# Performance work log

Hardware: AMD Instinct MI355X
Metric: run time of the kernel (lower is better)

The kernel has to match this reference:

```python
import jax, jax.numpy as jnp
import numpy as np

B, H, L, P = 16, 256, 4096, 64  # batch, d_input, seq len (= kernel_size), d_state
R_MIN, R_MAX = 0.9, 1.0         # strong_stability, weak_stability (discrete reservoir radii)


def _as_complex(x):
    # torch.view_as_complex equivalent: trailing dim 2 = (real, imag)
    return x[..., 0] + 1j * x[..., 1]


def setup_inputs() -> dict:
    key = jax.random.key(0)
    ks = jax.random.split(key, 6)
    u = jax.random.normal(ks[0], (B, H, L), jnp.float32)
    C = jax.random.normal(ks[1], (H, P, 2), jnp.float32)       # complex (H,P) as view_as_real
    D = jax.random.normal(ks[2], (H, H), jnp.float32)
    B_bar = jax.random.normal(ks[3], (P, H, 2), jnp.float32)   # complex (P,H) as view_as_real
    # DiscreteStateReservoir: eigenvalues with |lambda| in [strong, weak), uniform phase
    radius = jax.random.uniform(ks[4], (P,), jnp.float32, R_MIN, R_MAX)
    theta = jax.random.uniform(ks[5], (P,), jnp.float32, 0.0, 2.0 * np.pi)
    Lambda_bar = jnp.stack([radius * jnp.cos(theta), radius * jnp.sin(theta)], axis=-1)
    powers = jnp.arange(L, dtype=jnp.float32)
    return {"u": u, "C": C, "D": D, "B_bar": B_bar, "Lambda_bar": Lambda_bar, "powers": powers}


def reference(u, C, D, B_bar, Lambda_bar, powers):
    Cc = _as_complex(C)            # (H, P) complex64
    Bc = _as_complex(B_bar)        # (P, H) complex64
    Lc = _as_complex(Lambda_bar)   # (P,)   complex64
    # Vandermonde: (P, L) = Lambda_bar[p] ** powers[l]
    vand = Lc[:, None] ** powers[None, :]
    # einsum('hp,ph->hp') is elementwise C[h,p]*B_bar[p,h]; then contract over p
    kernel = jnp.einsum('hp,pl->hl', Cc * Bc.T, vand)            # (H, L) complex64
    # circular FFT convolution along L
    y = jnp.fft.ifft(jnp.fft.fft(u, axis=-1) * jnp.fft.fft(kernel, axis=-1)[None], axis=-1)
    # einsum('hh,bhl->bhl', D, u) uses only diag(D)
    y = y.real + jnp.diagonal(D)[None, :, None] * u
    return jnp.tanh(y)
```

## Files before the change

### kernel.cpp

```cpp
#include <hip/hip_runtime.h>
#include <cmath>

#define NF 4096
#define PI2F 6.2831853071795864769f

typedef float2 cf;

__device__ __forceinline__ cf cmulf(cf a, cf b){
  return make_float2(fmaf(a.x, b.x, -(a.y*b.y)), fmaf(a.x, b.y, a.y*b.x));
}
__device__ __forceinline__ cf cadd(cf a, cf b){ return make_float2(a.x+b.x, a.y+b.y); }
__device__ __forceinline__ cf csub(cf a, cf b){ return make_float2(a.x-b.x, a.y-b.y); }

__device__ __forceinline__ int phys8(int i){ return i + (i >> 3); }

__device__ __forceinline__ int rev8(int i){
  return ((i & 7) << 9) | (((i >> 3) & 7) << 6) | (((i >> 6) & 7) << 3) | ((i >> 9) & 7);
}

template<int INV>
__device__ __forceinline__ void dft8(cf* v){
  const float HF = 0.7071067811865476f;
  cf e0,e1,e2,e3,o0,o1,o2,o3;
  {
    cf t0 = cadd(v[0], v[4]);
    cf t1 = csub(v[0], v[4]);
    cf t2 = cadd(v[2], v[6]);
    cf t3 = csub(v[2], v[6]);
    e0 = cadd(t0,t2); e2 = csub(t0,t2);
    if (!INV){ e1 = make_float2(t1.x+t3.y, t1.y-t3.x); e3 = make_float2(t1.x-t3.y, t1.y+t3.x); }
    else     { e1 = make_float2(t1.x-t3.y, t1.y+t3.x); e3 = make_float2(t1.x+t3.y, t1.y-t3.x); }
  }
  {
    cf t0 = cadd(v[1], v[5]);
    cf t1 = csub(v[1], v[5]);
    cf t2 = cadd(v[3], v[7]);
    cf t3 = csub(v[3], v[7]);
    o0 = cadd(t0,t2); o2 = csub(t0,t2);
    if (!INV){ o1 = make_float2(t1.x+t3.y, t1.y-t3.x); o3 = make_float2(t1.x-t3.y, t1.y+t3.x); }
    else     { o1 = make_float2(t1.x-t3.y, t1.y+t3.x); o3 = make_float2(t1.x+t3.y, t1.y-t3.x); }
  }
  cf w1, w2, w3;
  if (!INV){
    w1 = make_float2(HF*(o1.x + o1.y), HF*(o1.y - o1.x));
    w2 = make_float2(o2.y, -o2.x);
    w3 = make_float2(HF*(o3.y - o3.x), -HF*(o3.x + o3.y));
  } else {
    w1 = make_float2(HF*(o1.x - o1.y), HF*(o1.y + o1.x));
    w2 = make_float2(-o2.y, o2.x);
    w3 = make_float2(-HF*(o3.x + o3.y), HF*(o3.x - o3.y));
  }
  v[0] = cadd(e0,o0); v[4] = csub(e0,o0);
  v[1] = cadd(e1,w1); v[5] = csub(e1,w1);
  v[2] = cadd(e2,w2); v[6] = csub(e2,w2);
  v[3] = cadd(e3,w3); v[7] = csub(e3,w3);
}

__device__ __forceinline__ void twiddle8(cf* v, float ang){
  float s, c;
  __sincosf(ang, &s, &c);
  float c2 = 2.0f * c;
  cf T[8];
  T[1] = make_float2(c, s);
  T[2] = make_float2(fmaf(c2, c, -1.0f), c2 * s);
#pragma unroll
  for (int r = 3; r < 8; ++r)
    T[r] = make_float2(fmaf(c2, T[r-1].x, -T[r-2].x), fmaf(c2, T[r-1].y, -T[r-2].y));
#pragma unroll
  for (int r = 1; r < 8; ++r) v[r] = cmulf(v[r], T[r]);
}

__device__ __forceinline__ float fast_tanh(float x){
  float e = __expf(2.0f*x);
  return 1.0f - __fdividef(2.0f, e + 1.0f);
}

__global__ void k_geo(const float* __restrict__ Lam, float4* __restrict__ tab){
  int gid = blockIdx.x*256 + threadIdx.x;
  int p = gid >> 12;
  int w = gid & 4095;
  int k = rev8(w);
  double lr = (double)Lam[2*p], li = (double)Lam[2*p+1];
  double r2 = lr*lr + li*li;
  double r  = sqrt(r2);
  double tt = atan2(li, lr) * 0.15915494309189535;
  double rN = exp2(4096.0 * (0.5 * log2(r2)));
  double pN = 4096.0 * tt;
  pN -= floor(pN);
  double sN, cN;
  sincospi(2.0*pN, &sN, &cN);
  double numr = 1.0 - rN*cN;
  double numi =     - rN*sN;
  double ph1 = tt - (double)k * (1.0/4096.0);
  double s1, c1; sincospi(2.0*ph1, &s1, &c1);
  double d1r = 1.0 - r*c1, d1i = -r*s1;
  double inv1 = 1.0/(d1r*d1r + d1i*d1i);
  double g1r = (numr*d1r + numi*d1i)*inv1;
  double g1i = (numi*d1r - numr*d1i)*inv1;
  double ph2 = tt + (double)k * (1.0/4096.0);
  double s2, c2; sincospi(2.0*ph2, &s2, &c2);
  double d2r = 1.0 - r*c2, d2i = -r*s2;
  double inv2 = 1.0/(d2r*d2r + d2i*d2i);
  double g2r = (numr*d2r + numi*d2i)*inv2;
  double g2i = (numi*d2r - numr*d2i)*inv2;
  const double hN = 0.5/4096.0;
  double Ar  =  (g1r + g2r)*hN, Ai  = (g1i - g2i)*hN;
  double B2r = -(g1i + g2i)*hN, B2i = (g1r - g2r)*hN;
  tab[(size_t)p*4096 + w] = make_float4((float)Ar, (float)Ai, (float)B2r, (float)B2i);
}

__global__ __launch_bounds__(512,4) void k_red(
    const float* __restrict__ C, const float* __restrict__ Bb,
    const float4* __restrict__ tab, const float* __restrict__ D,
    cf* __restrict__ M){
  __shared__ cf Wsh[32][64];
  __shared__ float4 Tt[8][128];
  const int t  = threadIdx.x;
  const int hg = blockIdx.x >> 5;
  const int ls = blockIdx.x & 31;
  const int h0 = hg*32;
  const int w0 = ls*128;
#pragma unroll
  for (int e = 0; e < 4; ++e){
    int idx = e*512 + t;
    int hl = idx >> 6, p = idx & 63;
    int h = h0 + hl;
    cf cc = ((const cf*)C)[h*64 + p];
    cf bb = ((const cf*)Bb)[p*256 + h];
    Wsh[hl][p] = cmulf(cc, bb);
  }
  const int wave = t >> 6;
  const int lane = t & 63;
  const int hh = wave*4;
  float accr[2][4] = {{0,0,0,0},{0,0,0,0}};
  float acci[2][4] = {{0,0,0,0},{0,0,0,0}};
  for (int pc = 0; pc < 8; ++pc){
    __syncthreads();
#pragma unroll
    for (int e = 0; e < 2; ++e){
      int idx = e*512 + t;
      int row = idx >> 7, col = idx & 127;
      Tt[row][col] = tab[(size_t)(pc*8 + row)*4096 + w0 + col];
    }
    __syncthreads();
#pragma unroll
    for (int p = 0; p < 8; ++p){
      cf Wc[4];
#pragma unroll
      for (int h = 0; h < 4; ++h) Wc[h] = Wsh[hh + h][pc*8 + p];
#pragma unroll
      for (int j = 0; j < 2; ++j){
        float4 f = Tt[p][lane + 64*j];
#pragma unroll
        for (int h = 0; h < 4; ++h){
          accr[j][h] = fmaf(Wc[h].x, f.x, fmaf(Wc[h].y, f.z, accr[j][h]));
          acci[j][h] = fmaf(Wc[h].x, f.y, fmaf(Wc[h].y, f.w, acci[j][h]));
        }
      }
    }
  }
  const float invN = 1.0f/4096.0f;
#pragma unroll
  for (int h = 0; h < 4; ++h){
    int hq = h0 + hh + h;
    float dd = D[hq*256 + hq] * invN;
#pragma unroll
    for (int j = 0; j < 2; ++j)
      M[(size_t)hq*NF + w0 + lane + 64*j] = make_float2(accr[j][h] + dd, acci[j][h]);
  }
}

__global__ __launch_bounds__(512,8) void k_main(
    const float* __restrict__ u, const cf* __restrict__ M, float* __restrict__ out){
  __shared__ cf X[4608];
  const int t  = threadIdx.x;
  const int h  = blockIdx.x >> 3;
  const int pr = blockIdx.x & 7;
  const size_t row0 = ((size_t)pr*256 + h)*(size_t)NF;
  const size_t row1 = row0 + (size_t)8*256*NF;
  const float* u0 = u + row0;
  const float* u1 = u + row1;
  cf v[8];
#pragma unroll
  for (int q = 0; q < 8; ++q) v[q] = make_float2(u0[t + 512*q], u1[t + 512*q]);
  dft8<0>(v);
  twiddle8(v, -(PI2F/4096.0f)*(float)t);
#pragma unroll
  for (int r = 0; r < 8; ++r) X[phys8(t + 512*r)] = v[r];
  __syncthreads();
  const int b2 = ((t >> 6) << 9) | (t & 63);
#pragma unroll
  for (int q = 0; q < 8; ++q) v[q] = X[phys8(b2 + 64*q)];
  dft8<0>(v);
  twiddle8(v, -(PI2F/512.0f)*(float)(t & 63));
#pragma unroll
  for (int r = 0; r < 8; ++r) X[phys8(b2 + 64*r)] = v[r];
  __syncthreads();
  const int b3 = ((t >> 3) << 6) | (t & 7);
#pragma unroll
  for (int q = 0; q < 8; ++q) v[q] = X[phys8(b3 + 8*q)];
  dft8<0>(v);
  twiddle8(v, -(PI2F/64.0f)*(float)(t & 7));
#pragma unroll
  for (int r = 0; r < 8; ++r) X[phys8(b3 + 8*r)] = v[r];
  __syncthreads();
  float4 mf0, mf1;
  {
    const float4* Mr = (const float4*)(M + (size_t)h*NF + 8*t);
    mf0 = Mr[0]; mf1 = Mr[1];
  }
#pragma unroll
  for (int q = 0; q < 8; ++q) v[q] = X[phys8(8*t + q)];
  dft8<0>(v);
  {
    const float4* Mr = (const float4*)(M + (size_t)h*NF + 8*t);
    float4 f2 = Mr[2], f3 = Mr[3];
    v[0] = cmulf(v[0], make_float2(mf0.x, mf0.y));
    v[1] = cmulf(v[1], make_float2(mf0.z, mf0.w));
    v[2] = cmulf(v[2], make_float2(mf1.x, mf1.y));
    v[3] = cmulf(v[3], make_float2(mf1.z, mf1.w));
    v[4] = cmulf(v[4], make_float2(f2.x, f2.y));
    v[5] = cmulf(v[5], make_float2(f2.z, f2.w));
    v[6] = cmulf(v[6], make_float2(f3.x, f3.y));
    v[7] = cmulf(v[7], make_float2(f3.z, f3.w));
  }
  dft8<1>(v);
#pragma unroll
  for (int q = 0; q < 8; ++q) X[phys8(8*t + q)] = v[q];
  __syncthreads();
#pragma unroll
  for (int r = 0; r < 8; ++r) v[r] = X[phys8(b3 + 8*r)];
  twiddle8(v, (PI2F/64.0f)*(float)(t & 7));
  dft8<1>(v);
#pragma unroll
  for (int q = 0; q < 8; ++q) X[phys8(b3 + 8*q)] = v[q];
  __syncthreads();
#pragma unroll
  for (int r = 0; r < 8; ++r) v[r] = X[phys8(b2 + 64*r)];
  twiddle8(v, (PI2F/512.0f)*(float)(t & 63));
  dft8<1>(v);
#pragma unroll
  for (int q = 0; q < 8; ++q) X[phys8(b2 + 64*q)] = v[q];
  __syncthreads();
#pragma unroll
  for (int r = 0; r < 8; ++r) v[r] = X[phys8(t + 512*r)];
  twiddle8(v, (PI2F/4096.0f)*(float)t);
  dft8<1>(v);
  float* o0 = out + row0;
  float* o1 = out + row1;
#pragma unroll
  for (int q = 0; q < 8; ++q){
    o0[t + 512*q] = fast_tanh(v[q].x);
    o1[t + 512*q] = fast_tanh(v[q].y);
  }
}

extern "C" void kernel_launch(void* const* d_in, const int* in_sizes, int n_in,
                              void* d_out, int out_size, void* d_ws, size_t ws_size,
                              hipStream_t stream){
  const float* u   = (const float*)d_in[0];
  const float* C   = (const float*)d_in[1];
  const float* D   = (const float*)d_in[2];
  const float* Bb  = (const float*)d_in[3];
  const float* Lam = (const float*)d_in[4];
  float* out = (float*)d_out;
  char* ws = (char*)d_ws;
  cf*     M   = (cf*)ws;
  float4* tab = (float4*)(ws + (size_t)(8u << 20));

  k_geo <<<dim3(1024), dim3(256), 0, stream>>>(Lam, tab);
  k_red <<<dim3(256),  dim3(512), 0, stream>>>(C, Bb, tab, D, M);
  k_main<<<dim3(2048), dim3(512), 0, stream>>>(u, M, out);
}
```

Measured before the change: 64.04 us.

## Compute geometric table in float with per-block shared setup; prefetch M early

```diff
diff --git a/kernel.cpp b/kernel.cpp
--- a/kernel.cpp
+++ b/kernel.cpp
@@ -75,38 +75,45 @@
   return 1.0f - __fdividef(2.0f, e + 1.0f);
 }
 
-__global__ void k_geo(const float* __restrict__ Lam, float4* __restrict__ tab){
-  int gid = blockIdx.x*256 + threadIdx.x;
-  int p = gid >> 12;
-  int w = gid & 4095;
-  int k = rev8(w);
-  double lr = (double)Lam[2*p], li = (double)Lam[2*p+1];
-  double r2 = lr*lr + li*li;
-  double r  = sqrt(r2);
-  double tt = atan2(li, lr) * 0.15915494309189535;
-  double rN = exp2(4096.0 * (0.5 * log2(r2)));
-  double pN = 4096.0 * tt;
-  pN -= floor(pN);
-  double sN, cN;
-  sincospi(2.0*pN, &sN, &cN);
-  double numr = 1.0 - rN*cN;
-  double numi =     - rN*sN;
-  double ph1 = tt - (double)k * (1.0/4096.0);
-  double s1, c1; sincospi(2.0*ph1, &s1, &c1);
-  double d1r = 1.0 - r*c1, d1i = -r*s1;
-  double inv1 = 1.0/(d1r*d1r + d1i*d1i);
-  double g1r = (numr*d1r + numi*d1i)*inv1;
-  double g1i = (numi*d1r - numr*d1i)*inv1;
-  double ph2 = tt + (double)k * (1.0/4096.0);
-  double s2, c2; sincospi(2.0*ph2, &s2, &c2);
-  double d2r = 1.0 - r*c2, d2i = -r*s2;
-  double inv2 = 1.0/(d2r*d2r + d2i*d2i);
-  double g2r = (numr*d2r + numi*d2i)*inv2;
-  double g2i = (numi*d2r - numr*d2i)*inv2;
-  const double hN = 0.5/4096.0;
-  double Ar  =  (g1r + g2r)*hN, Ai  = (g1i - g2i)*hN;
-  double B2r = -(g1i + g2i)*hN, B2i = (g1r - g2r)*hN;
-  tab[(size_t)p*4096 + w] = make_float4((float)Ar, (float)Ai, (float)B2r, (float)B2i);
+__global__ __launch_bounds__(1024) void k_geo(const float* __restrict__ Lam,
+                                              float4* __restrict__ tab){
+  __shared__ float sh[4];
+  const int p = blockIdx.x;
+  const int t = threadIdx.x;
+  if (t == 0){
+    double lr = (double)Lam[2*p], li = (double)Lam[2*p+1];
+    double r2 = lr*lr + li*li;
+    double tt = atan2(li, lr) * 0.15915494309189535;
+    double rN = exp2(4096.0 * (0.5 * log2(r2)));
+    double pN = 4096.0 * tt;  pN -= floor(pN);
+    double sN, cN;  sincospi(2.0*pN, &sN, &cN);
+    sh[0] = (float)tt;
+    sh[1] = (float)sqrt(r2);
+    sh[2] = (float)(1.0 - rN*cN);
+    sh[3] = (float)(-rN*sN);
+  }
+  __syncthreads();
+  const float tt = sh[0], r = sh[1], numr = sh[2], numi = sh[3];
+  const float hN = 0.5f/4096.0f;
+  float4* dst = tab + (size_t)p*4096;
+#pragma unroll
+  for (int s = 0; s < 4; ++s){
+    int w = s*1024 + t;
+    int k = rev8(w);
+    float kf = (float)k * (1.0f/4096.0f);
+    float s1, c1;  sincospif(2.0f*(tt - kf), &s1, &c1);
+    float d1r = fmaf(-r, c1, 1.0f), d1i = -r*s1;
+    float i1 = 1.0f / fmaf(d1r, d1r, d1i*d1i);
+    float g1r = (numr*d1r + numi*d1i)*i1;
+    float g1i = (numi*d1r - numr*d1i)*i1;
+    float s2, c2;  sincospif(2.0f*(tt + kf), &s2, &c2);
+    float d2r = fmaf(-r, c2, 1.0f), d2i = -r*s2;
+    float i2 = 1.0f / fmaf(d2r, d2r, d2i*d2i);
+    float g2r = (numr*d2r + numi*d2i)*i2;
+    float g2i = (numi*d2r - numr*d2i)*i2;
+    dst[w] = make_float4( (g1r + g2r)*hN, (g1i - g2i)*hN,
+                         -(g1i + g2i)*hN, (g1r - g2r)*hN);
+  }
 }
 
 __global__ __launch_bounds__(512,4) void k_red(
@@ -183,6 +190,8 @@
   cf v[8];
 #pragma unroll
   for (int q = 0; q < 8; ++q) v[q] = make_float2(u0[t + 512*q], u1[t + 512*q]);
+  const float4* Mr = (const float4*)(M + (size_t)h*NF + 8*t);
+  float4 mf0 = Mr[0], mf1 = Mr[1], mf2 = Mr[2], mf3 = Mr[3];
   dft8<0>(v);
   twiddle8(v, -(PI2F/4096.0f)*(float)t);
 #pragma unroll
@@ -204,26 +213,17 @@
 #pragma unroll
   for (int r = 0; r < 8; ++r) X[phys8(b3 + 8*r)] = v[r];
   __syncthreads();
-  float4 mf0, mf1;
-  {
-    const float4* Mr = (const float4*)(M + (size_t)h*NF + 8*t);
-    mf0 = Mr[0]; mf1 = Mr[1];
-  }
 #pragma unroll
   for (int q = 0; q < 8; ++q) v[q] = X[phys8(8*t + q)];
   dft8<0>(v);
-  {
-    const float4* Mr = (const float4*)(M + (size_t)h*NF + 8*t);
-    float4 f2 = Mr[2], f3 = Mr[3];
-    v[0] = cmulf(v[0], make_float2(mf0.x, mf0.y));
-    v[1] = cmulf(v[1], make_float2(mf0.z, mf0.w));
-    v[2] = cmulf(v[2], make_float2(mf1.x, mf1.y));
-    v[3] = cmulf(v[3], make_float2(mf1.z, mf1.w));
-    v[4] = cmulf(v[4], make_float2(f2.x, f2.y));
-    v[5] = cmulf(v[5], make_float2(f2.z, f2.w));
-    v[6] = cmulf(v[6], make_float2(f3.x, f3.y));
-    v[7] = cmulf(v[7], make_float2(f3.z, f3.w));
-  }
+  v[0] = cmulf(v[0], make_float2(mf0.x, mf0.y));
+  v[1] = cmulf(v[1], make_float2(mf0.z, mf0.w));
+  v[2] = cmulf(v[2], make_float2(mf1.x, mf1.y));
+  v[3] = cmulf(v[3], make_float2(mf1.z, mf1.w));
+  v[4] = cmulf(v[4], make_float2(mf2.x, mf2.y));
+  v[5] = cmulf(v[5], make_float2(mf2.z, mf2.w));
+  v[6] = cmulf(v[6], make_float2(mf3.x, mf3.y));
+  v[7] = cmulf(v[7], make_float2(mf3.z, mf3.w));
   dft8<1>(v);
 #pragma unroll
   for (int q = 0; q < 8; ++q) X[phys8(8*t + q)] = v[q];
@@ -268,7 +268,7 @@
   cf*     M   = (cf*)ws;
   float4* tab = (float4*)(ws + (size_t)(8u << 20));
 
-  k_geo <<<dim3(1024), dim3(256), 0, stream>>>(Lam, tab);
-  k_red <<<dim3(256),  dim3(512), 0, stream>>>(C, Bb, tab, D, M);
-  k_main<<<dim3(2048), dim3(512), 0, stream>>>(u, M, out);
-}
+  k_geo <<<dim3(64),   dim3(1024), 0, stream>>>(Lam, tab);
+  k_red <<<dim3(256),  dim3(512),  0, stream>>>(C, Bb, tab, D, M);
+  k_main<<<dim3(2048), dim3(512),  0, stream>>>(u, M, out);
+}
```

Result: slower. 96.24 us (+50.3%).
